# Kernel tuning notes

Hardware: AMD Instinct MI355X
Metric: run time of the kernel (lower is better)

The kernel has to match this reference:

```python
import jax, jax.numpy as jnp
import numpy as np

D_MODEL = 1024
N_HEADS = 16
HEAD_DIM = D_MODEL // N_HEADS
B, S = 2, 2048


def setup_inputs() -> dict:
    key = jax.random.key(0)
    ks = jax.random.split(key, 6)
    w_scale = 1.0 / np.sqrt(D_MODEL)
    return {
        "query": jax.random.normal(ks[0], (B, S, D_MODEL), dtype=jnp.float32),
        "Wq": jax.random.normal(ks[1], (D_MODEL, D_MODEL), dtype=jnp.float32) * w_scale,
        "Wk": jax.random.normal(ks[2], (D_MODEL, D_MODEL), dtype=jnp.float32) * w_scale,
        "Wv": jax.random.normal(ks[3], (D_MODEL, D_MODEL), dtype=jnp.float32) * w_scale,
        "Wo": jax.random.normal(ks[4], (D_MODEL, D_MODEL), dtype=jnp.float32) * w_scale,
        "bo": jnp.zeros((D_MODEL,), dtype=jnp.float32),
    }


def reference(query, Wq, Wk, Wv, Wo, bo):
    # Self-attention: key = value = query (forward() defaults).
    b, t, _ = query.shape
    # Q/K/V projections (nn.Linear applies x @ W.T; weights here are stored as
    # [out, in] like torch, so project with W.T). Split into heads: [B,H,T,Dh].
    def proj(x, W):
        return (x @ W.T).reshape(b, t, N_HEADS, HEAD_DIM).transpose(0, 2, 1, 3)

    q = proj(query, Wq)
    k = proj(query, Wk)
    v = proj(query, Wv)

    scale = 1.0 / np.sqrt(HEAD_DIM)
    scores = jnp.einsum("bhqd,bhkd->bhqk", q, k) * scale  # [B,H,T,T]
    # Causal mask (is_causal=True, not cross-attention).
    causal = jnp.tril(jnp.ones((t, t), dtype=bool))
    scores = jnp.where(causal, scores, jnp.finfo(scores.dtype).min)
    weights = jax.nn.softmax(scores, axis=-1)
    out = jnp.einsum("bhqk,bhkd->bhqd", weights, v)  # [B,H,T,Dh]
    out = out.transpose(0, 2, 1, 3).reshape(b, t, D_MODEL)
    # Output projection with bias (dropout is identity in eval mode).
    return out @ Wo.T + bo
```

## Files before the change

### kernel.cpp

```cpp
#include <hip/hip_runtime.h>
#include <hip/hip_bf16.h>
#include <math.h>

typedef __attribute__((ext_vector_type(8))) short short8;
typedef __attribute__((ext_vector_type(4))) float floatx4;
typedef __attribute__((ext_vector_type(2))) _Float16 half2v;
typedef __attribute__((ext_vector_type(4))) _Float16 half4v;

#define MFMA_BF16_32(a, b, c) __builtin_amdgcn_mfma_f32_16x16x32_bf16(a, b, c, 0, 0, 0)
#define MFMA_F16_16(a, b, c) __builtin_amdgcn_mfma_f32_16x16x16f16(a, b, c, 0, 0, 0)

static constexpr int NH = 16;
static constexpr int Bb = 2;
static constexpr int Ss = 2048;
static constexpr int DM = 1024;

__device__ inline unsigned short f2bf(float f) {
    unsigned int u = __float_as_uint(f);
    u += 0x7fffu + ((u >> 16) & 1u);
    return (unsigned short)(u >> 16);
}

__device__ __forceinline__ half2v pkrtz(float a, float b) {
    return __builtin_bit_cast(half2v, __builtin_amdgcn_cvt_pkrtz(a, b));
}

__device__ __forceinline__ void gload_lds16(const unsigned short* g, unsigned short* l) {
    __builtin_amdgcn_global_load_lds(
        (const __attribute__((address_space(1))) unsigned int*)g,
        (__attribute__((address_space(3))) unsigned int*)l, 16, 0, 0);
}

__global__ void convert_all(const float* __restrict__ X, const float* __restrict__ w0,
                            const float* __restrict__ w1, const float* __restrict__ w2,
                            const float* __restrict__ w3, unsigned short* __restrict__ dstX,
                            unsigned short* __restrict__ dstW) {
    const int bid = blockIdx.x;
    const float* src;
    unsigned short* dst;
    int i;
    if (bid < 4096) {
        src = X; dst = dstX; i = bid * 256 + threadIdx.x;
    } else {
        const int w = (bid - 4096) >> 10;
        src = (w == 0) ? w0 : (w == 1) ? w1 : (w == 2) ? w2 : w3;
        dst = dstW + (size_t)w * 1048576;
        i = ((bid - 4096) & 1023) * 256 + threadIdx.x;
    }
    float4 v = ((const float4*)src)[i];
    ushort4 o;
    o.x = f2bf(v.x); o.y = f2bf(v.y); o.z = f2bf(v.z); o.w = f2bf(v.w);
    ((ushort4*)dst)[i] = o;
}

__global__ __launch_bounds__(256) void gemm_qkv(const unsigned short* __restrict__ A,
                                                const unsigned short* __restrict__ Bm,
                                                unsigned short* __restrict__ Qp,
                                                unsigned short* __restrict__ Kp,
                                                unsigned short* __restrict__ Vt) {
    __shared__ __align__(16) unsigned short As[2][4096];
    __shared__ __align__(16) unsigned short Bs[2][4096];
    const int K = 1024;
    const int tid = threadIdx.x;
    const int wave = tid >> 6, lane = tid & 63;
    const int quad = lane >> 4, l16 = lane & 15;
    const int wr = wave >> 1, wc = wave & 1;
    const int bm = blockIdx.x * 128;
    const int by = blockIdx.y;
    const int bn = by * 128;

    const int s0 = wave * 64 + lane;
    const int srow = s0 >> 2;
    const int scg = (s0 & 3) ^ ((srow >> 1) & 3);
    const unsigned short* gA0 = A + (size_t)(bm + srow) * K + scg * 8;
    const unsigned short* gB0 = Bm + (size_t)(bn + srow) * K + scg * 8;

    auto stage = [&](int k0, int buf) {
        gload_lds16(gA0 + k0, &As[buf][wave * 512]);
        gload_lds16(gA0 + (size_t)64 * K + k0, &As[buf][2048 + wave * 512]);
        gload_lds16(gB0 + k0, &Bs[buf][wave * 512]);
        gload_lds16(gB0 + (size_t)64 * K + k0, &Bs[buf][2048 + wave * 512]);
    };

    floatx4 acc[4][4];
#pragma unroll
    for (int i = 0; i < 4; i++)
#pragma unroll
        for (int j = 0; j < 4; j++) acc[i][j] = (floatx4)0.0f;

    stage(0, 0);
    int buf = 0;
    for (int k0 = 0; k0 < K; k0 += 32) {
        __syncthreads();
        if (k0 + 32 < K) stage(k0 + 32, buf ^ 1);
        short8 af[4];
#pragma unroll
        for (int im = 0; im < 4; im++) {
            const int frow = wr * 64 + im * 16 + l16;
            af[im] = *(const short8*)&As[buf][frow * 32 + ((quad ^ ((frow >> 1) & 3)) * 8)];
        }
#pragma unroll
        for (int jn = 0; jn < 4; jn++) {
            const int frow = wc * 64 + jn * 16 + l16;
            short8 bf = *(const short8*)&Bs[buf][frow * 32 + ((quad ^ ((frow >> 1) & 3)) * 8)];
#pragma unroll
            for (int im = 0; im < 4; im++) acc[im][jn] = MFMA_BF16_32(af[im], bf, acc[im][jn]);
        }
        buf ^= 1;
    }
    __syncthreads();

    unsigned short* LB = &As[0][0];

    if (by < 16) {
        unsigned short* dst = (by < 8) ? Qp : Kp;
        const int nb = (by & 7) * 128;
        const float scale = (by < 8) ? 0.125f : 1.0f;
#pragma unroll
        for (int hf = 0; hf < 2; ++hf) {
            if (wc == hf) {
#pragma unroll
                for (int im = 0; im < 4; im++)
#pragma unroll
                    for (int jn = 0; jn < 4; jn++) {
                        const int row = wr * 64 + im * 16 + quad * 4;
                        const int col = jn * 16 + l16;
#pragma unroll
                        for (int r = 0; r < 4; r++)
                            LB[(row + r) * 64 + col] = f2bf(acc[im][jn][r] * scale);
                    }
            }
            __syncthreads();
#pragma unroll
            for (int i = 0; i < 4; ++i) {
                const int flat = i * 256 + tid;
                const int row = flat >> 3, ch = flat & 7;
                short8 v = *(const short8*)&LB[row * 64 + ch * 8];
                *(short8*)&dst[(size_t)(bm + row) * 1024 + nb + hf * 64 + ch * 8] = v;
            }
            __syncthreads();
        }
    } else {
        _Float16* LF = (_Float16*)LB;
        const int dbase = (by - 16) * 128;
        const int bI = bm >> 11, sbase = bm & 2047;
#pragma unroll
        for (int hf = 0; hf < 2; ++hf) {
            if (wc == hf) {
#pragma unroll
                for (int im = 0; im < 4; im++)
#pragma unroll
                    for (int jn = 0; jn < 4; jn++) {
                        const int d64 = jn * 16 + l16;
                        const int sl = wr * 64 + im * 16 + quad * 4;
                        *(half2v*)&LF[d64 * 128 + sl] = pkrtz(acc[im][jn][0], acc[im][jn][1]);
                        *(half2v*)&LF[d64 * 128 + sl + 2] = pkrtz(acc[im][jn][2], acc[im][jn][3]);
                    }
            }
            __syncthreads();
#pragma unroll
            for (int i = 0; i < 4; ++i) {
                const int flat = i * 256 + tid;
                const int dr = flat >> 4, ch = flat & 15;
                short8 v = *(const short8*)&LF[dr * 128 + ch * 8];
                const int d = dbase + hf * 64 + dr;
                const int head = d >> 6, d64g = d & 63;
                *(short8*)&Vt[(((size_t)(bI * 16 + head)) * 64 + d64g) * 2048 + sbase + ch * 8] = v;
            }
            __syncthreads();
        }
    }
}

__global__ __launch_bounds__(256) void gemm_out(const unsigned short* __restrict__ A,
                                                const unsigned short* __restrict__ Bm,
                                                float* __restrict__ C,
                                                const float* __restrict__ bias) {
    __shared__ __align__(16) unsigned short As[2][4096];
    __shared__ __align__(16) unsigned short Bs[2][2048];
    const int K = 1024;
    const int tid = threadIdx.x;
    const int wave = tid >> 6, lane = tid & 63;
    const int quad = lane >> 4, l16 = lane & 15;
    const int bm = blockIdx.x * 128, bn = blockIdx.y * 64;

    const int s0 = wave * 64 + lane;
    const int srow = s0 >> 2;
    const int scg = (s0 & 3) ^ ((srow >> 1) & 3);
    const unsigned short* gA0 = A + (size_t)(bm + srow) * K + scg * 8;
    const unsigned short* gB0 = Bm + (size_t)(bn + srow) * K + scg * 8;

    auto stage = [&](int k0, int buf) {
        gload_lds16(gA0 + k0, &As[buf][wave * 512]);
        gload_lds16(gA0 + (size_t)64 * K + k0, &As[buf][2048 + wave * 512]);
        gload_lds16(gB0 + k0, &Bs[buf][wave * 512]);
    };

    floatx4 acc[2][4];
#pragma unroll
    for (int i = 0; i < 2; i++)
#pragma unroll
        for (int j = 0; j < 4; j++) acc[i][j] = (floatx4)0.0f;

    stage(0, 0);
    int buf = 0;
    for (int k0 = 0; k0 < K; k0 += 32) {
        __syncthreads();
        if (k0 + 32 < K) stage(k0 + 32, buf ^ 1);
        short8 af[2];
#pragma unroll
        for (int im = 0; im < 2; im++) {
            const int frow = wave * 32 + im * 16 + l16;
            af[im] = *(const short8*)&As[buf][frow * 32 + ((quad ^ ((frow >> 1) & 3)) * 8)];
        }
#pragma unroll
        for (int jn = 0; jn < 4; jn++) {
            const int frow = jn * 16 + l16;
            short8 bf = *(const short8*)&Bs[buf][frow * 32 + ((quad ^ ((frow >> 1) & 3)) * 8)];
#pragma unroll
            for (int im = 0; im < 2; im++) acc[im][jn] = MFMA_BF16_32(af[im], bf, acc[im][jn]);
        }
        buf ^= 1;
    }

#pragma unroll
    for (int im = 0; im < 2; im++) {
#pragma unroll
        for (int jn = 0; jn < 4; jn++) {
            const int row0 = bm + wave * 32 + im * 16 + quad * 4;
            const int colg = bn + jn * 16 + l16;
            const float bv = bias[colg];
#pragma unroll
            for (int r = 0; r < 4; r++)
                C[(size_t)(row0 + r) * 1024 + colg] = acc[im][jn][r] + bv;
        }
    }
}

__global__ __launch_bounds__(256) void flash_attn(const unsigned short* __restrict__ Qp,
                                                  const unsigned short* __restrict__ Kp,
                                                  const _Float16* __restrict__ Vt,
                                                  unsigned short* __restrict__ Out) {
    __shared__ __align__(16) unsigned short Ks[2][4096];
    __shared__ __align__(16) _Float16 Vs[2][4096];
    const int bx = blockIdx.x, h = blockIdx.y, b = blockIdx.z;
    int qt = (bx + h) & 15;
    if (b) qt = 15 - qt;
    const int tid = threadIdx.x, w = tid >> 6, lane = tid & 63;
    const int quad = lane >> 4, l16 = lane & 15;

    const int t8 = tid >> 3;
    const int cg = (tid & 7) ^ (t8 & 7);
    const unsigned short* gK0 = Kp + ((size_t)(b * 2048 + t8) << 10) + h * 64 + cg * 8;
    const unsigned short* gK1 = gK0 + ((size_t)32 << 10);
    const _Float16* gV0 = Vt + ((size_t)((b * 16 + h) * 64 + t8) << 11) + cg * 8;
    const _Float16* gV1 = gV0 + ((size_t)32 << 11);
    unsigned short* ldsK = &Ks[0][0] + w * 512;
    _Float16* ldsV = &Vs[0][0] + w * 512;

    auto stage = [&](int kt, int buf) {
        const size_t ko = (size_t)kt << 16;
        const size_t vo = (size_t)kt << 6;
        gload_lds16(gK0 + ko, ldsK + buf * 4096);
        gload_lds16(gK1 + ko, ldsK + buf * 4096 + 2048);
        gload_lds16((const unsigned short*)(gV0 + vo), (unsigned short*)(ldsV + buf * 4096));
        gload_lds16((const unsigned short*)(gV1 + vo), (unsigned short*)(ldsV + buf * 4096 + 2048));
    };

    stage(0, 0);

    short8 qfA[2], qfB[2];
    {
        const unsigned short* qa =
            Qp + ((size_t)(b * 2048 + qt * 128 + w * 16 + l16) << 10) + h * 64 + quad * 8;
        qfA[0] = *(const short8*)qa;
        qfA[1] = *(const short8*)(qa + 32);
        const unsigned short* qb = qa + ((size_t)64 << 10);
        qfB[0] = *(const short8*)qb;
        qfB[1] = *(const short8*)(qb + 32);
    }

    floatx4 accA[4], accB[4];
#pragma unroll
    for (int dt = 0; dt < 4; dt++) { accA[dt] = (floatx4)0.0f; accB[dt] = (floatx4)0.0f; }
    float lA = 0.0f, lB = 0.0f;
    const int qloc = w * 16 + l16;
    const int sw = l16 & 7;
    const int ktEnd = 2 * qt + 1;

    for (int kt = 0; kt <= ktEnd; ++kt) {
        __syncthreads();
        const int buf = kt & 1;
        if (kt < ktEnd) stage(kt + 1, buf ^ 1);
        const bool aAct = (kt <= 2 * qt);
        const bool aDiag = (kt == 2 * qt);
        const bool bDiag = (kt == ktEnd);
        const unsigned short* KB = &Ks[buf][0];
        const _Float16* VB = &Vs[buf][0];

#pragma unroll
        for (int sc = 0; sc < 4; ++sc) {
            const int rowk = sc * 16 + l16;
            short8 kf0 = *(const short8*)&KB[rowk * 64 + ((quad ^ sw) * 8)];
            short8 kf1 = *(const short8*)&KB[rowk * 64 + (((4 + quad) ^ sw) * 8)];

            half4v pA, pB;
            if (aAct) {
                floatx4 sA = MFMA_BF16_32(kf0, qfA[0], (floatx4)(-2.0f));
                sA = MFMA_BF16_32(kf1, qfA[1], sA);
                float ps[4];
#pragma unroll
                for (int r = 0; r < 4; ++r) {
                    float e = __expf(sA[r]);
                    if (aDiag && (sc * 16 + quad * 4 + r > qloc)) e = 0.0f;
                    ps[r] = e;
                }
                lA += (ps[0] + ps[1]) + (ps[2] + ps[3]);
                pA = __builtin_shufflevector(pkrtz(ps[0], ps[1]), pkrtz(ps[2], ps[3]), 0, 1, 2, 3);
            }
            {
                floatx4 sB = MFMA_BF16_32(kf0, qfB[0], (floatx4)(-2.0f));
                sB = MFMA_BF16_32(kf1, qfB[1], sB);
                float ps[4];
#pragma unroll
                for (int r = 0; r < 4; ++r) {
                    float e = __expf(sB[r]);
                    if (bDiag && (sc * 16 + quad * 4 + r > qloc)) e = 0.0f;
                    ps[r] = e;
                }
                lB += (ps[0] + ps[1]) + (ps[2] + ps[3]);
                pB = __builtin_shufflevector(pkrtz(ps[0], ps[1]), pkrtz(ps[2], ps[3]), 0, 1, 2, 3);
            }

#pragma unroll
            for (int dt = 0; dt < 4; ++dt) {
                const int rowv = dt * 16 + l16;
                const int cgv = ((sc * 2 + (quad >> 1)) ^ sw);
                half4v vf = *(const half4v*)&VB[rowv * 64 + cgv * 8 + (quad & 1) * 4];
                if (aAct) accA[dt] = MFMA_F16_16(vf, pA, accA[dt]);
                accB[dt] = MFMA_F16_16(vf, pB, accB[dt]);
            }
        }
    }

    lA += __shfl_xor(lA, 16); lA += __shfl_xor(lA, 32);
    lB += __shfl_xor(lB, 16); lB += __shfl_xor(lB, 32);
    const float iA = 1.0f / lA;
    const float iB = 1.0f / lB;

    const size_t rowA = (size_t)(b * 2048 + qt * 128 + w * 16 + l16);
    const size_t rowB = rowA + 64;
#pragma unroll
    for (int dt = 0; dt < 4; ++dt) {
        const int col = h * 64 + dt * 16 + quad * 4;
        ushort4 oa, ob;
        oa.x = f2bf(accA[dt][0] * iA); oa.y = f2bf(accA[dt][1] * iA);
        oa.z = f2bf(accA[dt][2] * iA); oa.w = f2bf(accA[dt][3] * iA);
        ob.x = f2bf(accB[dt][0] * iB); ob.y = f2bf(accB[dt][1] * iB);
        ob.z = f2bf(accB[dt][2] * iB); ob.w = f2bf(accB[dt][3] * iB);
        *(ushort4*)&Out[rowA * 1024 + col] = oa;
        *(ushort4*)&Out[rowB * 1024 + col] = ob;
    }
}

extern "C" void kernel_launch(void* const* d_in, const int* in_sizes, int n_in,
                              void* d_out, int out_size, void* d_ws, size_t ws_size,
                              hipStream_t stream) {
    const float* X  = (const float*)d_in[0];
    const float* Wq = (const float*)d_in[1];
    const float* Wk = (const float*)d_in[2];
    const float* Wv = (const float*)d_in[3];
    const float* Wo = (const float*)d_in[4];
    const float* bo = (const float*)d_in[5];

    unsigned short* ws = (unsigned short*)d_ws;
    unsigned short* Xb   = ws;
    unsigned short* W4   = ws + (size_t)4194304;
    unsigned short* Wob  = W4 + (size_t)3145728;
    unsigned short* Qp   = ws + (size_t)8388608;
    unsigned short* Kp   = ws + (size_t)12582912;
    unsigned short* Vt   = ws + (size_t)16777216;
    unsigned short* At   = ws + (size_t)20971520;

    convert_all<<<8192, 256, 0, stream>>>(X, Wq, Wk, Wv, Wo, Xb, W4);

    gemm_qkv<<<dim3(32, 24), 256, 0, stream>>>(Xb, W4, Qp, Kp, Vt);

    flash_attn<<<dim3(16, NH, Bb), 256, 0, stream>>>(Qp, Kp, (const _Float16*)Vt, At);

    gemm_out<<<dim3(32, 16), 256, 0, stream>>>(At, Wob, (float*)d_out, bo);
}
```

Measured before the change: 205.3 us.

## Remap GEMM blocks per XCD for L2 locality and deepen gemm_out K-step

Both GEMMs now launch a 1D grid and remap block IDs so that blocks scheduled on the same XCD (round-robin l&7) cover a compact 8xN sub-tile of the output. Neighbouring blocks that share A/B panels should then hit the same L2. gemm_out also doubles its K step per iteration from 32 to 64, staging two K-halves per buffer. That halves the barrier count but doubles its LDS footprint, which may reduce occupancy.

```diff
diff --git a/kernel.cpp b/kernel.cpp
--- a/kernel.cpp
+++ b/kernel.cpp
@@ -65,8 +65,12 @@
     const int wave = tid >> 6, lane = tid & 63;
     const int quad = lane >> 4, l16 = lane & 15;
     const int wr = wave >> 1, wc = wave & 1;
-    const int bm = blockIdx.x * 128;
-    const int by = blockIdx.y;
+
+    const int l = blockIdx.x;
+    const int xcd = l & 7, slot = l >> 3;
+    const int bx = (xcd & 3) * 8 + (slot & 7);
+    const int by = (xcd >> 2) * 12 + (slot >> 3);
+    const int bm = bx * 128;
     const int bn = by * 128;
 
     const int s0 = wave * 64 + lane;
@@ -176,13 +180,18 @@
                                                 const unsigned short* __restrict__ Bm,
                                                 float* __restrict__ C,
                                                 const float* __restrict__ bias) {
-    __shared__ __align__(16) unsigned short As[2][4096];
-    __shared__ __align__(16) unsigned short Bs[2][2048];
+    __shared__ __align__(16) unsigned short As[2][8192];
+    __shared__ __align__(16) unsigned short Bs[2][4096];
     const int K = 1024;
     const int tid = threadIdx.x;
     const int wave = tid >> 6, lane = tid & 63;
     const int quad = lane >> 4, l16 = lane & 15;
-    const int bm = blockIdx.x * 128, bn = blockIdx.y * 64;
+
+    const int l = blockIdx.x;
+    const int xcd = l & 7, slot = l >> 3;
+    const int bx = (xcd & 3) * 8 + (slot & 7);
+    const int by = (xcd >> 2) * 8 + (slot >> 3);
+    const int bm = bx * 128, bn = by * 64;
 
     const int s0 = wave * 64 + lane;
     const int srow = s0 >> 2;
@@ -191,9 +200,13 @@
     const unsigned short* gB0 = Bm + (size_t)(bn + srow) * K + scg * 8;
 
     auto stage = [&](int k0, int buf) {
-        gload_lds16(gA0 + k0, &As[buf][wave * 512]);
-        gload_lds16(gA0 + (size_t)64 * K + k0, &As[buf][2048 + wave * 512]);
-        gload_lds16(gB0 + k0, &Bs[buf][wave * 512]);
+#pragma unroll
+        for (int kh = 0; kh < 2; ++kh) {
+            gload_lds16(gA0 + k0 + kh * 32, &As[buf][kh * 4096 + wave * 512]);
+            gload_lds16(gA0 + (size_t)64 * K + k0 + kh * 32,
+                        &As[buf][kh * 4096 + 2048 + wave * 512]);
+            gload_lds16(gB0 + k0 + kh * 32, &Bs[buf][kh * 2048 + wave * 512]);
+        }
     };
 
     floatx4 acc[2][4];
@@ -204,21 +217,27 @@
 
     stage(0, 0);
     int buf = 0;
-    for (int k0 = 0; k0 < K; k0 += 32) {
+    for (int k0 = 0; k0 < K; k0 += 64) {
         __syncthreads();
-        if (k0 + 32 < K) stage(k0 + 32, buf ^ 1);
-        short8 af[2];
-#pragma unroll
-        for (int im = 0; im < 2; im++) {
-            const int frow = wave * 32 + im * 16 + l16;
-            af[im] = *(const short8*)&As[buf][frow * 32 + ((quad ^ ((frow >> 1) & 3)) * 8)];
-        }
-#pragma unroll
-        for (int jn = 0; jn < 4; jn++) {
-            const int frow = jn * 16 + l16;
-            short8 bf = *(const short8*)&Bs[buf][frow * 32 + ((quad ^ ((frow >> 1) & 3)) * 8)];
-#pragma unroll
-            for (int im = 0; im < 2; im++) acc[im][jn] = MFMA_BF16_32(af[im], bf, acc[im][jn]);
+        if (k0 + 64 < K) stage(k0 + 64, buf ^ 1);
+#pragma unroll
+        for (int kh = 0; kh < 2; ++kh) {
+            const int abase = kh * 4096, bbase = kh * 2048;
+            short8 af[2];
+#pragma unroll
+            for (int im = 0; im < 2; im++) {
+                const int frow = wave * 32 + im * 16 + l16;
+                af[im] = *(const short8*)&As[buf][abase + frow * 32 +
+                                                  ((quad ^ ((frow >> 1) & 3)) * 8)];
+            }
+#pragma unroll
+            for (int jn = 0; jn < 4; jn++) {
+                const int frow = jn * 16 + l16;
+                short8 bf = *(const short8*)&Bs[buf][bbase + frow * 32 +
+                                                     ((quad ^ ((frow >> 1) & 3)) * 8)];
+#pragma unroll
+                for (int im = 0; im < 2; im++) acc[im][jn] = MFMA_BF16_32(af[im], bf, acc[im][jn]);
+            }
         }
         buf ^= 1;
     }
@@ -384,9 +403,9 @@
 
     convert_all<<<8192, 256, 0, stream>>>(X, Wq, Wk, Wv, Wo, Xb, W4);
 
-    gemm_qkv<<<dim3(32, 24), 256, 0, stream>>>(Xb, W4, Qp, Kp, Vt);
+    gemm_qkv<<<768, 256, 0, stream>>>(Xb, W4, Qp, Kp, Vt);
 
     flash_attn<<<dim3(16, NH, Bb), 256, 0, stream>>>(Qp, Kp, (const _Float16*)Vt, At);
 
-    gemm_out<<<dim3(32, 16), 256, 0, stream>>>(At, Wob, (float*)d_out, bo);
-}
+    gemm_out<<<512, 256, 0, stream>>>(At, Wob, (float*)d_out, bo);
+}
```

New measurement: 200.8 us. 2.2% less time.
